# Optimization experiments

Hardware: AMD Instinct MI355X
Metric: run time of the kernel (lower is better)

Reference implementation:

```python
import jax, jax.numpy as jnp
import numpy as np

B, T, FEAT, IN = 32, 96, 2048, 4096  # batch, frames, feature_len, inshape (cat mode)


def setup_inputs() -> dict:
    key = jax.random.key(0)
    ks = jax.random.split(key, 12)
    s = 1.0 / np.sqrt(FEAT)  # PyTorch LSTMCell/Linear init scale ~ U(-1/sqrt(hidden), ...)
    f32 = jnp.float32
    return {
        "feature": jax.random.normal(ks[0], (B, T, IN), f32),
        "gumbel_u": jax.random.uniform(ks[1], (T - 1, B, 2), f32),
        "W_ih": jax.random.normal(ks[2], (4 * FEAT, IN), f32) * s,
        "b_ih": jax.random.normal(ks[3], (4 * FEAT,), f32) * s,
        "W_hh": jax.random.normal(ks[4], (4 * FEAT, FEAT), f32) * s,
        "b_hh": jax.random.normal(ks[5], (4 * FEAT,), f32) * s,
        "W_pred": jax.random.normal(ks[6], (2, FEAT), f32) * s,
        "b_pred": jax.random.normal(ks[7], (2,), f32) * s,
        "W_util": jax.random.normal(ks[8], (1, FEAT), f32) * s,
        "b_util": jax.random.normal(ks[9], (1,), f32) * s,
        "W_use": jax.random.normal(ks[10], (2, FEAT), f32) * s,
        "b_use": jax.random.normal(ks[11], (2,), f32) * s,
    }


def reference(feature, gumbel_u, W_ih, b_ih, W_hh, b_hh,
              W_pred, b_pred, W_util, b_util, W_use, b_use):
    tau = 1.0
    eps = 1e-10
    x = jnp.transpose(feature, (1, 0, 2))          # [T, B, IN]
    gnoise = -jnp.log(-jnp.log(gumbel_u + eps) + eps)  # Gumbel(0,1), [T-1, B, 2]

    def lstm_cell(x_t, h, c):
        gates = x_t @ W_ih.T + b_ih + h @ W_hh.T + b_hh  # [B, 4F]
        i, f, g, o = jnp.split(gates, 4, axis=-1)        # PyTorch gate order i,f,g,o
        c2 = jax.nn.sigmoid(f) * c + jax.nn.sigmoid(i) * jnp.tanh(g)
        h2 = jax.nn.sigmoid(o) * jnp.tanh(c2)
        return h2, c2

    def heads(h):
        return h @ W_pred.T + b_pred, h @ W_util.T + b_util

    h0 = jnp.zeros((x.shape[1], FEAT), x.dtype)
    h, c = lstm_cell(x[0], h0, h0)                   # step 0: no gating
    pred0, util0 = heads(h)

    def step(carry, inp):
        h_prev, c_prev = carry
        x_t, g_t = inp
        h_new, c2 = lstm_cell(x_t, h_prev, c_prev)
        logits = h_new @ W_use.T + b_use             # [B, 2]
        use = jax.nn.softmax((logits + g_t) / tau, axis=-1)  # soft gumbel-softmax
        # bmm(stack([h_prev, h_new], -1), use) == convex mix of the two states
        h2 = h_prev * use[:, :1] + h_new * use[:, 1:2]
        pred, util = heads(h2)
        return (h2, c2), (pred, util)

    _, (preds, utils) = jax.lax.scan(step, (h, c), (x[1:], gnoise))
    pred = jnp.concatenate([pred0[None], preds], axis=0)   # [T, B, 2]
    util = jnp.concatenate([util0[None], utils], axis=0)   # [T, B, 1]
    return pred, util
```

## Files before the change

kernel.cpp:

```cpp
#include <hip/hip_runtime.h>
#include <cstdint>
#include <cstddef>

#define TT 96
#define BB 32
#define FEATD 2048
#define IND 4096
#define NG 8192
#define MROWS 3072

typedef _Float16 half8 __attribute__((ext_vector_type(8)));
typedef _Float16 half4 __attribute__((ext_vector_type(4)));
typedef _Float16 half2v __attribute__((ext_vector_type(2)));
typedef float f32x4 __attribute__((ext_vector_type(4)));

#define WS_FEAT16 0u
#define WS_HBUF   0u
#define WS_WIH16  25165824u
#define WS_WHH16  92274688u
#define WS_PRE16  125829120u
#define WS_GAB    176160768u
#define WS_HD     176185344u
#define WS_BAR    176222208u

#define NWG 256
#define BAR_WORDS 8192

__global__ void __launch_bounds__(256) k_convert(
    const float* __restrict__ feat, const float* __restrict__ wih,
    const float* __restrict__ whh,
    _Float16* __restrict__ feat16, _Float16* __restrict__ wih16,
    _Float16* __restrict__ whh16, unsigned* __restrict__ flags)
{
  size_t id = (size_t)blockIdx.x * blockDim.x + threadIdx.x;
  size_t stride = (size_t)gridDim.x * blockDim.x;
  for (size_t i = id; i < (size_t)MROWS * IND / 4; i += stride) {
    f32x4 v = ((const f32x4*)feat)[i];
    half4 h = { (_Float16)v[0], (_Float16)v[1], (_Float16)v[2], (_Float16)v[3] };
    ((half4*)feat16)[i] = h;
  }
  for (size_t i = id; i < (size_t)NG * IND / 4; i += stride) {
    f32x4 v = ((const f32x4*)wih)[i];
    half4 h = { (_Float16)v[0], (_Float16)v[1], (_Float16)v[2], (_Float16)v[3] };
    ((half4*)wih16)[i] = h;
  }
  for (size_t i = id; i < (size_t)NG * FEATD / 4; i += stride) {
    f32x4 v = ((const f32x4*)whh)[i];
    half4 h = { (_Float16)v[0], (_Float16)v[1], (_Float16)v[2], (_Float16)v[3] };
    ((half4*)whh16)[i] = h;
  }
  for (size_t i = id; i < BAR_WORDS; i += stride) flags[i] = 0u;
}

__device__ __forceinline__ void gload16(const _Float16* g, _Float16* l) {
  __builtin_amdgcn_global_load_lds(
      (const __attribute__((address_space(1))) void*)g,
      (__attribute__((address_space(3))) void*)l, 16, 0, 0);
}

#define GBUF 49152

__global__ void __launch_bounds__(512, 1) k_gemm2(
    const _Float16* __restrict__ A,
    const _Float16* __restrict__ Bw,
    const float* __restrict__ bih, const float* __restrict__ bhh,
    _Float16* __restrict__ C)
{
  extern __shared__ __align__(16) char smem[];
  const int tid = threadIdx.x;
  const int l = tid & 63;
  const int wv = tid >> 6;
  const int wm = wv >> 1, wn = wv & 1;
  const int rr = l & 15;

  const int lin = blockIdx.x;
  const int sw = (lin & 7) * 96 + (lin >> 3);
  const int bx = sw & 63;
  const int by = sw >> 6;
  const int mbase = by * 256;
  const int nbase = bx * 128;

  const _Float16* Ablk = A + (size_t)mbase * IND;
  const _Float16* Bblk = Bw + (size_t)nbase * IND;

  const int gdat = (l & 3) ^ ((l >> 3) & 3);
  const _Float16* gptr[3];
  int ldsk0[3], ldsk1[3];
#pragma unroll
  for (int j = 0; j < 3; ++j) {
    int c = wv * 3 + j;
    bool isA = (c < 16);
    int rowbase = isA ? c * 16 : (c - 16) * 16;
    gptr[j] = (isA ? Ablk : Bblk) + (size_t)(rowbase + (l >> 2)) * IND + gdat * 8;
    ldsk0[j] = (isA ? 0 : 32768) + rowbase * 64;
    ldsk1[j] = (isA ? 16384 : 32768 + 8192) + rowbase * 64;
  }

  const int gpos = (l >> 4) ^ ((rr >> 1) & 3);
  int offA[4], offB[4];
#pragma unroll
  for (int f = 0; f < 4; ++f) {
    offA[f] = (wm * 64 + f * 16 + rr) * 64 + gpos * 16;
    offB[f] = (wn * 64 + f * 16 + rr) * 64 + gpos * 16;
  }

  f32x4 acc[4][4] = {};

#pragma unroll
  for (int j = 0; j < 3; ++j) gload16(gptr[j], (_Float16*)(smem + ldsk0[j]));
#pragma unroll
  for (int j = 0; j < 3; ++j) gload16(gptr[j] + 32, (_Float16*)(smem + ldsk1[j]));
  asm volatile("s_waitcnt vmcnt(3)" ::: "memory");
  asm volatile("s_barrier" ::: "memory");

#pragma unroll 1
  for (int tt = 0; tt < 64; ++tt) {
    const char* cb = smem + (tt & 1) * GBUF;
    char* nb = (char*)smem + ((tt & 1) ^ 1) * GBUF;
    const int kt1 = (tt + 1) * 64;

    {
      half8 af[4], bf[4];
#pragma unroll
      for (int f = 0; f < 4; ++f) af[f] = *(const half8*)(cb + offA[f]);
#pragma unroll
      for (int f = 0; f < 4; ++f) bf[f] = *(const half8*)(cb + 32768 + offB[f]);
      if (tt < 63) {
#pragma unroll
        for (int j = 0; j < 3; ++j)
          gload16(gptr[j] + kt1, (_Float16*)(nb + ldsk0[j]));
        asm volatile("s_waitcnt vmcnt(3)" ::: "memory");
      } else {
        asm volatile("s_waitcnt vmcnt(0)" ::: "memory");
      }
      asm volatile("s_barrier" ::: "memory");
      __builtin_amdgcn_s_setprio(1);
#pragma unroll
      for (int fm = 0; fm < 4; ++fm)
#pragma unroll
        for (int fn = 0; fn < 4; ++fn)
          acc[fm][fn] = __builtin_amdgcn_mfma_f32_16x16x32_f16(af[fm], bf[fn], acc[fm][fn], 0, 0, 0);
      __builtin_amdgcn_s_setprio(0);
      asm volatile("s_barrier" ::: "memory");
    }
    {
      half8 af[4], bf[4];
#pragma unroll
      for (int f = 0; f < 4; ++f) af[f] = *(const half8*)(cb + 16384 + offA[f]);
#pragma unroll
      for (int f = 0; f < 4; ++f) bf[f] = *(const half8*)(cb + 32768 + 8192 + offB[f]);
      if (tt < 63) {
#pragma unroll
        for (int j = 0; j < 3; ++j)
          gload16(gptr[j] + kt1 + 32, (_Float16*)(nb + ldsk1[j]));
        asm volatile("s_waitcnt vmcnt(3)" ::: "memory");
      }
      asm volatile("s_barrier" ::: "memory");
      __builtin_amdgcn_s_setprio(1);
#pragma unroll
      for (int fm = 0; fm < 4; ++fm)
#pragma unroll
        for (int fn = 0; fn < 4; ++fn)
          acc[fm][fn] = __builtin_amdgcn_mfma_f32_16x16x32_f16(af[fm], bf[fn], acc[fm][fn], 0, 0, 0);
      __builtin_amdgcn_s_setprio(0);
      asm volatile("s_barrier" ::: "memory");
    }
  }

#pragma unroll
  for (int fn = 0; fn < 4; ++fn) {
    int n = nbase + wn * 64 + fn * 16 + (l & 15);
    float bias = bih[n] + bhh[n];
#pragma unroll
    for (int fm = 0; fm < 4; ++fm) {
      int m0 = mbase + wm * 64 + fm * 16 + (l >> 4) * 4;
#pragma unroll
      for (int r = 0; r < 4; ++r)
        C[(size_t)(m0 + r) * NG + n] = (_Float16)(acc[fm][fn][r] + bias);
    }
  }
}

#define LDS_WHH 0
#define LDS_RED 131072
#define RED_STRIDE_F 1152
#define LDS_TOTAL 149504

__device__ __forceinline__ float fast_sigmoid(float x) {
  return 1.f / (1.f + __expf(-x));
}
__device__ __forceinline__ float fast_tanh(float x) {
  return 1.f - 2.f / (__expf(2.f * x) + 1.f);
}

__global__ void __launch_bounds__(512, 1) k_recur(
    const float* __restrict__ gumbel,
    const float* __restrict__ Wuse, const float* __restrict__ buse,
    const _Float16* __restrict__ whh16,
    const _Float16* __restrict__ pre16,
    _Float16* __restrict__ hbuf,
    float* __restrict__ gab,
    unsigned* __restrict__ flags)
{
  extern __shared__ __align__(16) char smem[];
  const int tid = threadIdx.x;
  const int wg = blockIdx.x;
  const int wave = tid >> 6, lane = tid & 63;
  float* RED = (float*)(smem + LDS_RED);

  {
    int c = tid >> 4;
    int grow = (c >> 3) * FEATD + wg * 8 + (c & 7);
    const _Float16* src = whh16 + (size_t)grow * FEATD;
    char* dst = smem + LDS_WHH + c * 4096;
    int x = c & 7;
    for (int i = 0; i < 16; ++i) {
      int g = (tid & 15) + i * 16;
      *(half8*)(dst + ((g ^ x) << 4)) = *(const half8*)(src + g * 8);
    }
  }

  const int rr = lane & 15;
  const int lk = (lane >> 4) * 8;
  half8 uq0[8], uq1[8];
#pragma unroll
  for (int s = 0; s < 8; ++s) {
    int kk = wave * 256 + s * 32 + lk;
#pragma unroll
    for (int e = 0; e < 8; ++e) {
      uq0[s][e] = (_Float16)Wuse[kk + e];
      uq1[s][e] = (_Float16)Wuse[FEATD + kk + e];
    }
  }

  const int b_ = tid >> 3, fi_ = tid & 7;
  const float bq0 = buse[0], bq1 = buse[1];

  float G0 = 0.f, G1 = 0.f, G2 = 0.f, G3 = 0.f, cc = 0.f;
  const _Float16* prbase = pre16 + ((size_t)b_ * TT) * NG + wg * 8 + fi_;
  _Float16 pf0 = 0, pf1 = 0, pf2 = 0, pf3 = 0;
  _Float16 pn0 = 0, pn1 = 0, pn2 = 0, pn3 = 0;
  float gmc0 = 0.f, gmc1 = 0.f, gmn0 = 0.f, gmn1 = 0.f;
  if (tid < 256) {
    pf0 = prbase[0]; pf1 = prbase[FEATD]; pf2 = prbase[2 * FEATD]; pf3 = prbase[3 * FEATD];
  }
  __syncthreads();

  for (int t = 0; t < TT; ++t) {
    if (tid < 256 && t + 1 < TT) {
      const _Float16* p = prbase + (size_t)(t + 1) * NG;
      pn0 = p[0]; pn1 = p[FEATD]; pn2 = p[2 * FEATD]; pn3 = p[3 * FEATD];
      gmn0 = gumbel[(size_t)t * 64 + b_ * 2 + 0];
      gmn1 = gumbel[(size_t)t * 64 + b_ * 2 + 1];
    }
    if (tid < 256) {
      float ig = fast_sigmoid((float)pf0 + G0);
      float fg = fast_sigmoid((float)pf1 + G1);
      float gg = fast_tanh((float)pf2 + G2);
      float og = fast_sigmoid((float)pf3 + G3);
      cc = fg * cc + ig * gg;
      float hn = og * fast_tanh(cc);
      float hn_o = __shfl_xor(hn, 1);
      if ((fi_ & 1) == 0) {
        union { _Float16 h[2]; unsigned u; } pk;
        pk.h[0] = (_Float16)hn; pk.h[1] = (_Float16)hn_o;
        unsigned* dst = (unsigned*)(hbuf + (size_t)t * (BB * FEATD) + b_ * FEATD + wg * 8 + fi_);
        __hip_atomic_store(dst, pk.u, __ATOMIC_RELAXED, __HIP_MEMORY_SCOPE_AGENT);
      }
    }
    __syncthreads();
    const unsigned tgt = (unsigned)(t + 1);
    if (tid == 0)
      __hip_atomic_store(&flags[wg * 16], tgt, __ATOMIC_RELAXED, __HIP_MEMORY_SCOPE_AGENT);
    if (wg == 0) {
      if (wave == 0) {
        for (;;) {
          bool ok = true;
#pragma unroll
          for (int j = 0; j < 4; ++j) {
            unsigned v = __hip_atomic_load(&flags[(lane * 4 + j) * 16],
                                           __ATOMIC_RELAXED, __HIP_MEMORY_SCOPE_AGENT);
            ok &= (v >= tgt);
          }
          if (__all(ok)) break;
          __builtin_amdgcn_s_sleep(1);
        }
#pragma unroll
        for (int j = 0; j < 4; ++j)
          __hip_atomic_store(&flags[4096 + (lane * 4 + j) * 16], tgt,
                             __ATOMIC_RELAXED, __HIP_MEMORY_SCOPE_AGENT);
      }
    } else {
      if (tid == 0) {
        while (__hip_atomic_load(&flags[4096 + wg * 16],
                                 __ATOMIC_RELAXED, __HIP_MEMORY_SCOPE_AGENT) < tgt)
          __builtin_amdgcn_s_sleep(1);
      }
    }
    __syncthreads();

    const _Float16* hb = hbuf + (size_t)t * (BB * FEATD);
    f32x4 acc[2][2] = {};
    float q0a = 0.f, q1a = 0.f, q0b = 0.f, q1b = 0.f;
    {
      const int c0 = rr, c1 = 16 + rr;
      const char* wsl = smem + LDS_WHH;
#pragma unroll
      for (int s = 0; s < 8; ++s) {
        int kk = wave * 256 + s * 32 + lk;
        half8 a0 = *(const half8*)(hb + rr * FEATD + kk);
        half8 a1 = *(const half8*)(hb + (16 + rr) * FEATD + kk);
        int g = kk >> 3;
        half8 b0 = *(const half8*)(wsl + c0 * 4096 + ((g ^ (c0 & 7)) << 4));
        half8 b1 = *(const half8*)(wsl + c1 * 4096 + ((g ^ (c1 & 7)) << 4));
        acc[0][0] = __builtin_amdgcn_mfma_f32_16x16x32_f16(a0, b0, acc[0][0], 0, 0, 0);
        acc[0][1] = __builtin_amdgcn_mfma_f32_16x16x32_f16(a0, b1, acc[0][1], 0, 0, 0);
        acc[1][0] = __builtin_amdgcn_mfma_f32_16x16x32_f16(a1, b0, acc[1][0], 0, 0, 0);
        acc[1][1] = __builtin_amdgcn_mfma_f32_16x16x32_f16(a1, b1, acc[1][1], 0, 0, 0);
        const half2v* a0p = (const half2v*)&a0;
        const half2v* a1p = (const half2v*)&a1;
        const half2v* u0p = (const half2v*)&uq0[s];
        const half2v* u1p = (const half2v*)&uq1[s];
#pragma unroll
        for (int e = 0; e < 4; ++e) {
          q0a = __builtin_amdgcn_fdot2(a0p[e], u0p[e], q0a, false);
          q1a = __builtin_amdgcn_fdot2(a0p[e], u1p[e], q1a, false);
          q0b = __builtin_amdgcn_fdot2(a1p[e], u0p[e], q0b, false);
          q1b = __builtin_amdgcn_fdot2(a1p[e], u1p[e], q1b, false);
        }
      }
    }
    q0a += __shfl_xor(q0a, 16); q0a += __shfl_xor(q0a, 32);
    q1a += __shfl_xor(q1a, 16); q1a += __shfl_xor(q1a, 32);
    q0b += __shfl_xor(q0b, 16); q0b += __shfl_xor(q0b, 32);
    q1b += __shfl_xor(q1b, 16); q1b += __shfl_xor(q1b, 32);
    if (lane < 16) {
      float* pads = RED + (wave & 3) * RED_STRIDE_F + 32 + (wave >> 2) * 2;
      pads[rr * 36 + 0] = q0a; pads[rr * 36 + 1] = q1a;
      pads[(16 + rr) * 36 + 0] = q0b; pads[(16 + rr) * 36 + 1] = q1b;
    }
    {
      const int bb0 = (lane >> 4) * 4;
      const int cc0 = lane & 15;
      if (wave >= 4) {
        float* s0 = RED + (wave - 4) * RED_STRIDE_F;
        for (int fm = 0; fm < 2; ++fm)
          for (int fn = 0; fn < 2; ++fn)
            *(f32x4*)(s0 + (fn * 16 + cc0) * 36 + fm * 16 + bb0) = acc[fm][fn];
      }
      __syncthreads();
      if (wave < 4) {
        float* s0 = RED + wave * RED_STRIDE_F;
        for (int fm = 0; fm < 2; ++fm)
          for (int fn = 0; fn < 2; ++fn) {
            acc[fm][fn] += *(f32x4*)(s0 + (fn * 16 + cc0) * 36 + fm * 16 + bb0);
            *(f32x4*)(s0 + (fn * 16 + cc0) * 36 + fm * 16 + bb0) = acc[fm][fn];
          }
      }
      __syncthreads();
    }
    if (tid < 256) {
      float ga = 0.f, gb = 1.f;
      if (t > 0) {
        float q0 = bq0, q1 = bq1;
#pragma unroll
        for (int s2 = 0; s2 < 4; ++s2) {
          const float* pp = RED + s2 * RED_STRIDE_F + b_ * 36 + 32;
          q0 += pp[0] + pp[2]; q1 += pp[1] + pp[3];
        }
        float n0 = -logf(-logf(gmc0 + 1e-10f) + 1e-10f);
        float n1 = -logf(-logf(gmc1 + 1e-10f) + 1e-10f);
        float l0 = q0 + n0;
        float l1 = q1 + n1;
        float mx = fmaxf(l0, l1);
        float e0 = __expf(l0 - mx), e1 = __expf(l1 - mx);
        float inv = 1.f / (e0 + e1);
        ga = e0 * inv; gb = e1 * inv;
        if (wg == 0 && fi_ == 0) {
          gab[(t * BB + b_) * 2 + 0] = ga;
          gab[(t * BB + b_) * 2 + 1] = gb;
        }
      }
      {
        const int base = fi_ * 36 + b_;
        float m0 = RED[base] + RED[RED_STRIDE_F + base] + RED[2 * RED_STRIDE_F + base] + RED[3 * RED_STRIDE_F + base];
        float m1 = RED[base + 8 * 36] + RED[RED_STRIDE_F + base + 8 * 36] + RED[2 * RED_STRIDE_F + base + 8 * 36] + RED[3 * RED_STRIDE_F + base + 8 * 36];
        float m2 = RED[base + 16 * 36] + RED[RED_STRIDE_F + base + 16 * 36] + RED[2 * RED_STRIDE_F + base + 16 * 36] + RED[3 * RED_STRIDE_F + base + 16 * 36];
        float m3 = RED[base + 24 * 36] + RED[RED_STRIDE_F + base + 24 * 36] + RED[2 * RED_STRIDE_F + base + 24 * 36] + RED[3 * RED_STRIDE_F + base + 24 * 36];
        G0 = ga * G0 + gb * m0;
        G1 = ga * G1 + gb * m1;
        G2 = ga * G2 + gb * m2;
        G3 = ga * G3 + gb * m3;
      }
      pf0 = pn0; pf1 = pn1; pf2 = pn2; pf3 = pn3;
      gmc0 = gmn0; gmc1 = gmn1;
    }
  }
}

__global__ void __launch_bounds__(256) k_heads(
    const _Float16* __restrict__ hbuf,
    const float* __restrict__ Wpred, const float* __restrict__ Wutil,
    float* __restrict__ hd)
{
  const int t = blockIdx.x;
  const int tid = threadIdx.x;
  const int b = tid >> 3, fi = tid & 7;
  const _Float16* h = hbuf + ((size_t)t * BB + b) * FEATD;
  float d0 = 0.f, d1 = 0.f, d2 = 0.f;
  for (int j = 0; j < 32; ++j) {
    int k = fi * 8 + j * 64;
    half8 v = *(const half8*)(h + k);
#pragma unroll
    for (int e = 0; e < 8; ++e) {
      float x = (float)v[e];
      d0 += x * Wpred[k + e];
      d1 += x * Wpred[FEATD + k + e];
      d2 += x * Wutil[k + e];
    }
  }
  for (int m = 1; m < 8; m <<= 1) {
    d0 += __shfl_xor(d0, m); d1 += __shfl_xor(d1, m); d2 += __shfl_xor(d2, m);
  }
  if (fi == 0) {
    float* o = hd + ((size_t)t * BB + b) * 3;
    o[0] = d0; o[1] = d1; o[2] = d2;
  }
}

__global__ void __launch_bounds__(64) k_scan(
    const float* __restrict__ hd,
    const float* __restrict__ gab,
    const float* __restrict__ bpred, const float* __restrict__ butil,
    float* __restrict__ out)
{
  const int b = threadIdx.x;
  if (b >= BB) return;
  const float bp0 = bpred[0], bp1 = bpred[1], bu0 = butil[0];
  float L0 = hd[b * 3 + 0], L1 = hd[b * 3 + 1], L2 = hd[b * 3 + 2];
  out[b * 2 + 0] = L0 + bp0;
  out[b * 2 + 1] = L1 + bp1;
  out[TT * BB * 2 + b] = L2 + bu0;
  for (int t = 1; t < TT; ++t) {
    float ga = gab[(t * BB + b) * 2 + 0];
    float gb = gab[(t * BB + b) * 2 + 1];
    const float* d = hd + ((size_t)t * BB + b) * 3;
    L0 = ga * L0 + gb * d[0];
    L1 = ga * L1 + gb * d[1];
    L2 = ga * L2 + gb * d[2];
    out[(t * BB + b) * 2 + 0] = L0 + bp0;
    out[(t * BB + b) * 2 + 1] = L1 + bp1;
    out[TT * BB * 2 + t * BB + b] = L2 + bu0;
  }
}

extern "C" void kernel_launch(void* const* d_in, const int* in_sizes, int n_in,
                              void* d_out, int out_size, void* d_ws, size_t ws_size,
                              hipStream_t stream) {
  const float* feat  = (const float*)d_in[0];
  const float* gumb  = (const float*)d_in[1];
  const float* Wih   = (const float*)d_in[2];
  const float* bih   = (const float*)d_in[3];
  const float* Whh   = (const float*)d_in[4];
  const float* bhh   = (const float*)d_in[5];
  const float* Wpred = (const float*)d_in[6];
  const float* bpred = (const float*)d_in[7];
  const float* Wutil = (const float*)d_in[8];
  const float* butil = (const float*)d_in[9];
  const float* Wuse  = (const float*)d_in[10];
  const float* buse  = (const float*)d_in[11];

  char* ws = (char*)d_ws;
  _Float16* feat16 = (_Float16*)(ws + WS_FEAT16);
  _Float16* hbufp  = (_Float16*)(ws + WS_HBUF);
  _Float16* wih16  = (_Float16*)(ws + WS_WIH16);
  _Float16* whh16  = (_Float16*)(ws + WS_WHH16);
  _Float16* pre16  = (_Float16*)(ws + WS_PRE16);
  float*    gabp   = (float*)(ws + WS_GAB);
  float*    hdp    = (float*)(ws + WS_HD);
  unsigned* flagp  = (unsigned*)(ws + WS_BAR);

  (void)in_sizes; (void)n_in; (void)out_size; (void)ws_size;

  hipFuncSetAttribute((const void*)k_gemm2,
                      hipFuncAttributeMaxDynamicSharedMemorySize, 2 * GBUF);
  hipFuncSetAttribute((const void*)k_recur,
                      hipFuncAttributeMaxDynamicSharedMemorySize, LDS_TOTAL);

  k_convert<<<2048, 256, 0, stream>>>(feat, Wih, Whh, feat16, wih16, whh16, flagp);
  k_gemm2<<<768, 512, 2 * GBUF, stream>>>(feat16, wih16, bih, bhh, pre16);
  k_recur<<<NWG, 512, LDS_TOTAL, stream>>>(gumb, Wuse, buse, whh16, pre16,
                                           hbufp, gabp, flagp);
  k_heads<<<TT, 256, 0, stream>>>(hbufp, Wpred, Wutil, hdp);
  k_scan<<<1, 64, 0, stream>>>(hdp, gabp, bpred, butil, (float*)d_out);
}
```

Measured before the change: 1.015 ms.

## Triple-buffer GEMM K-loop and fuse W_hh fp16 conversion into recurrence load

The input-projection GEMM moves from double to triple LDS buffering, prefetching two K-tiles ahead with adjusted waitcnt thresholds so global loads have more time to land. Separately, the W_hh fp32-to-fp16 conversion pass is removed from the convert kernel. The recurrence kernel now reads fp32 W_hh directly and converts while filling its LDS slice, saving one full write and read of the converted matrix. The GEMM now needs 144KB of LDS per workgroup, and the recurrence prologue reads twice as many bytes.

After: 960.7 us, median of 2. 1.06x faster.

```diff
diff --git a/kernel.cpp b/kernel.cpp
--- a/kernel.cpp
+++ b/kernel.cpp
@@ -17,7 +17,6 @@
 #define WS_FEAT16 0u
 #define WS_HBUF   0u
 #define WS_WIH16  25165824u
-#define WS_WHH16  92274688u
 #define WS_PRE16  125829120u
 #define WS_GAB    176160768u
 #define WS_HD     176185344u
@@ -28,9 +27,8 @@
 
 __global__ void __launch_bounds__(256) k_convert(
     const float* __restrict__ feat, const float* __restrict__ wih,
-    const float* __restrict__ whh,
     _Float16* __restrict__ feat16, _Float16* __restrict__ wih16,
-    _Float16* __restrict__ whh16, unsigned* __restrict__ flags)
+    unsigned* __restrict__ flags)
 {
   size_t id = (size_t)blockIdx.x * blockDim.x + threadIdx.x;
   size_t stride = (size_t)gridDim.x * blockDim.x;
@@ -44,11 +42,6 @@
     half4 h = { (_Float16)v[0], (_Float16)v[1], (_Float16)v[2], (_Float16)v[3] };
     ((half4*)wih16)[i] = h;
   }
-  for (size_t i = id; i < (size_t)NG * FEATD / 4; i += stride) {
-    f32x4 v = ((const f32x4*)whh)[i];
-    half4 h = { (_Float16)v[0], (_Float16)v[1], (_Float16)v[2], (_Float16)v[3] };
-    ((half4*)whh16)[i] = h;
-  }
   for (size_t i = id; i < BAR_WORDS; i += stride) flags[i] = 0u;
 }
 
@@ -59,6 +52,7 @@
 }
 
 #define GBUF 49152
+#define GLDS_TOTAL (3 * GBUF)
 
 __global__ void __launch_bounds__(512, 1) k_gemm2(
     const _Float16* __restrict__ A,
@@ -107,17 +101,21 @@
   f32x4 acc[4][4] = {};
 
 #pragma unroll
-  for (int j = 0; j < 3; ++j) gload16(gptr[j], (_Float16*)(smem + ldsk0[j]));
+  for (int j = 0; j < 3; ++j) gload16(gptr[j],      (_Float16*)(smem + ldsk0[j]));
 #pragma unroll
   for (int j = 0; j < 3; ++j) gload16(gptr[j] + 32, (_Float16*)(smem + ldsk1[j]));
-  asm volatile("s_waitcnt vmcnt(3)" ::: "memory");
+#pragma unroll
+  for (int j = 0; j < 3; ++j) gload16(gptr[j] + 64, (_Float16*)(smem + GBUF + ldsk0[j]));
+#pragma unroll
+  for (int j = 0; j < 3; ++j) gload16(gptr[j] + 96, (_Float16*)(smem + GBUF + ldsk1[j]));
+  asm volatile("s_waitcnt vmcnt(9)" ::: "memory");
   asm volatile("s_barrier" ::: "memory");
 
 #pragma unroll 1
   for (int tt = 0; tt < 64; ++tt) {
-    const char* cb = smem + (tt & 1) * GBUF;
-    char* nb = (char*)smem + ((tt & 1) ^ 1) * GBUF;
-    const int kt1 = (tt + 1) * 64;
+    const char* cb = smem + (tt % 3) * GBUF;
+    char* nb = (char*)smem + ((tt + 2) % 3) * GBUF;
+    const int kt2 = (tt + 2) * 64;
 
     {
       half8 af[4], bf[4];
@@ -125,11 +123,11 @@
       for (int f = 0; f < 4; ++f) af[f] = *(const half8*)(cb + offA[f]);
 #pragma unroll
       for (int f = 0; f < 4; ++f) bf[f] = *(const half8*)(cb + 32768 + offB[f]);
-      if (tt < 63) {
+      if (tt < 62) {
 #pragma unroll
         for (int j = 0; j < 3; ++j)
-          gload16(gptr[j] + kt1, (_Float16*)(nb + ldsk0[j]));
-        asm volatile("s_waitcnt vmcnt(3)" ::: "memory");
+          gload16(gptr[j] + kt2, (_Float16*)(nb + ldsk0[j]));
+        asm volatile("s_waitcnt vmcnt(9)" ::: "memory");
       } else {
         asm volatile("s_waitcnt vmcnt(0)" ::: "memory");
       }
@@ -149,11 +147,13 @@
       for (int f = 0; f < 4; ++f) af[f] = *(const half8*)(cb + 16384 + offA[f]);
 #pragma unroll
       for (int f = 0; f < 4; ++f) bf[f] = *(const half8*)(cb + 32768 + 8192 + offB[f]);
-      if (tt < 63) {
+      if (tt < 62) {
 #pragma unroll
         for (int j = 0; j < 3; ++j)
-          gload16(gptr[j] + kt1 + 32, (_Float16*)(nb + ldsk1[j]));
-        asm volatile("s_waitcnt vmcnt(3)" ::: "memory");
+          gload16(gptr[j] + kt2 + 32, (_Float16*)(nb + ldsk1[j]));
+        asm volatile("s_waitcnt vmcnt(9)" ::: "memory");
+      } else {
+        asm volatile("s_waitcnt vmcnt(0)" ::: "memory");
       }
       asm volatile("s_barrier" ::: "memory");
       __builtin_amdgcn_s_setprio(1);
@@ -196,7 +196,7 @@
 __global__ void __launch_bounds__(512, 1) k_recur(
     const float* __restrict__ gumbel,
     const float* __restrict__ Wuse, const float* __restrict__ buse,
-    const _Float16* __restrict__ whh16,
+    const float* __restrict__ whh,
     const _Float16* __restrict__ pre16,
     _Float16* __restrict__ hbuf,
     float* __restrict__ gab,
@@ -211,12 +211,16 @@
   {
     int c = tid >> 4;
     int grow = (c >> 3) * FEATD + wg * 8 + (c & 7);
-    const _Float16* src = whh16 + (size_t)grow * FEATD;
+    const float* src = whh + (size_t)grow * FEATD;
     char* dst = smem + LDS_WHH + c * 4096;
     int x = c & 7;
     for (int i = 0; i < 16; ++i) {
       int g = (tid & 15) + i * 16;
-      *(half8*)(dst + ((g ^ x) << 4)) = *(const half8*)(src + g * 8);
+      f32x4 v0 = *(const f32x4*)(src + g * 8);
+      f32x4 v1 = *(const f32x4*)(src + g * 8 + 4);
+      half8 h = { (_Float16)v0[0], (_Float16)v0[1], (_Float16)v0[2], (_Float16)v0[3],
+                  (_Float16)v1[0], (_Float16)v1[1], (_Float16)v1[2], (_Float16)v1[3] };
+      *(half8*)(dst + ((g ^ x) << 4)) = h;
     }
   }
 
@@ -474,7 +478,6 @@
   _Float16* feat16 = (_Float16*)(ws + WS_FEAT16);
   _Float16* hbufp  = (_Float16*)(ws + WS_HBUF);
   _Float16* wih16  = (_Float16*)(ws + WS_WIH16);
-  _Float16* whh16  = (_Float16*)(ws + WS_WHH16);
   _Float16* pre16  = (_Float16*)(ws + WS_PRE16);
   float*    gabp   = (float*)(ws + WS_GAB);
   float*    hdp    = (float*)(ws + WS_HD);
@@ -483,13 +486,13 @@
   (void)in_sizes; (void)n_in; (void)out_size; (void)ws_size;
 
   hipFuncSetAttribute((const void*)k_gemm2,
-                      hipFuncAttributeMaxDynamicSharedMemorySize, 2 * GBUF);
+                      hipFuncAttributeMaxDynamicSharedMemorySize, GLDS_TOTAL);
   hipFuncSetAttribute((const void*)k_recur,
                       hipFuncAttributeMaxDynamicSharedMemorySize, LDS_TOTAL);
 
-  k_convert<<<2048, 256, 0, stream>>>(feat, Wih, Whh, feat16, wih16, whh16, flagp);
-  k_gemm2<<<768, 512, 2 * GBUF, stream>>>(feat16, wih16, bih, bhh, pre16);
-  k_recur<<<NWG, 512, LDS_TOTAL, stream>>>(gumb, Wuse, buse, whh16, pre16,
+  k_convert<<<2048, 256, 0, stream>>>(feat, Wih, feat16, wih16, flagp);
+  k_gemm2<<<768, 512, GLDS_TOTAL, stream>>>(feat16, wih16, bih, bhh, pre16);
+  k_recur<<<NWG, 512, LDS_TOTAL, stream>>>(gumb, Wuse, buse, Whh, pre16,
                                            hbufp, gabp, flagp);
   k_heads<<<TT, 256, 0, stream>>>(hbufp, Wpred, Wutil, hdp);
   k_scan<<<1, 64, 0, stream>>>(hdp, gabp, bpred, butil, (float*)d_out);
```
